# Optimization experiments

Hardware: AMD Instinct MI355X
Metric: run time of the kernel (lower is better)

The kernel has to match this reference:

```python
import jax, jax.numpy as jnp
import numpy as np

B, LQ, LK, E, H = 2, 1024, 10000, 256, 8
D = E // H  # head_dim = 32


def setup_inputs() -> dict:
    key = jax.random.key(0)
    ks = jax.random.split(key, 10)
    s = 1.0 / np.sqrt(E).astype(np.float32)
    return {
        "bev_emb": jax.random.normal(ks[0], (B, LK, E), jnp.float32),
        "queries": jax.random.normal(ks[1], (B, LQ, E), jnp.float32),
        "Wq": jax.random.normal(ks[2], (E, E), jnp.float32) * s,
        "bq": jax.random.normal(ks[3], (E,), jnp.float32) * 0.01,
        "Wk": jax.random.normal(ks[4], (E, E), jnp.float32) * s,
        "bk": jax.random.normal(ks[5], (E,), jnp.float32) * 0.01,
        "Wv": jax.random.normal(ks[6], (E, E), jnp.float32) * s,
        "bv": jax.random.normal(ks[7], (E,), jnp.float32) * 0.01,
        "Wo": jax.random.normal(ks[8], (E, E), jnp.float32) * s,
        "bo": jax.random.normal(ks[9], (E,), jnp.float32) * 0.01,
    }


def reference(bev_emb, queries, Wq, bq, Wk, bk, Wv, bv, Wo, bo):
    Bn, Lq, Em = queries.shape
    Lk = bev_emb.shape[1]
    q = (queries @ Wq + bq).reshape(Bn, Lq, H, D)
    k = (bev_emb @ Wk + bk).reshape(Bn, Lk, H, D)
    v = (bev_emb @ Wv + bv).reshape(Bn, Lk, H, D)
    # NOTE: source applies no 1/sqrt(head_dim) scaling
    energy = jnp.einsum('bqhd,bkhd->bhqk', q, k)  # [B,H,Lq,Lk]
    attn = jax.nn.softmax(energy, axis=-1)
    out = jnp.einsum('bhqk,bkhd->bqhd', attn, v).reshape(Bn, Lq, Em)
    return out @ Wo + bo
```

## Files before the change

### kernel.cpp

```cpp
#include <hip/hip_runtime.h>
#include <hip/hip_bf16.h>

#define B_  2
#define LQ_ 1024
#define LK_ 10000
#define E_  256
#define H_  8
#define D_  32
#define NT_ ((LK_ + 63) / 64)
#define KVBLKS_ 625
#define QBLKS_  64

typedef __attribute__((ext_vector_type(8))) short bf16x8;
typedef __attribute__((ext_vector_type(4))) short bf16x4;
typedef __attribute__((ext_vector_type(4))) float f32x4;

#define LOG2E 1.4426950408889634f

static __device__ __forceinline__ short bfc(float x) {
  __bf16 b = (__bf16)x;
  return __builtin_bit_cast(short, b);
}
static __device__ __forceinline__ float bf2f(short s) {
  return (float)__builtin_bit_cast(__bf16, s);
}

#if __has_builtin(__builtin_amdgcn_exp2f)
static __device__ __forceinline__ float ex2(float x) {
  return __builtin_amdgcn_exp2f(x);
}
#else
static __device__ __forceinline__ float ex2(float x) { return exp2f(x); }
#endif

#if __has_builtin(__builtin_amdgcn_mfma_f32_16x16x16bf16_1k)
static __device__ __forceinline__ f32x4 mfma_pv(bf16x4 a, bf16x4 b, f32x4 c) {
  return __builtin_amdgcn_mfma_f32_16x16x16bf16_1k(a, b, c, 0, 0, 0);
}
#else
static __device__ __forceinline__ f32x4 mfma_pv(bf16x4 a, bf16x4 b, f32x4 c) {
  asm volatile("s_nop 1\n\tv_mfma_f32_16x16x16_bf16 %0, %1, %2, %0"
               : "+v"(c) : "v"(a), "v"(b));
  return c;
}
#endif

static __device__ __forceinline__ void tile_barrier() {
  __builtin_amdgcn_sched_barrier(0);
  asm volatile("s_waitcnt lgkmcnt(0)" ::: "memory");
  __builtin_amdgcn_s_barrier();
  __builtin_amdgcn_sched_barrier(0);
}

static __device__ __forceinline__ int xcd_swizzle(int flat, int nwg) {
  const int xcd = flat & 7, rest = flat >> 3;
  const int q = nwg >> 3, r = nwg & 7;
  return (xcd < r ? xcd * (q + 1) : r * (q + 1) + (xcd - r) * q) + rest;
}

static __device__ __forceinline__ void split8(const float4& a, const float4& b,
                                              bf16x8& hi, bf16x8& lo) {
  float v[8] = {a.x, a.y, a.z, a.w, b.x, b.y, b.z, b.w};
#pragma unroll
  for (int i = 0; i < 8; ++i) {
    const short h = bfc(v[i]);
    hi[i] = h;
    lo[i] = bfc(v[i] - bf2f(h));
  }
}

__global__ __launch_bounds__(256) void wtrans4(
    const float* __restrict__ W0, const float* __restrict__ W1,
    const float* __restrict__ W2, const float* __restrict__ W3,
    unsigned short* __restrict__ T0, unsigned short* __restrict__ T1,
    unsigned short* __restrict__ T2, unsigned short* __restrict__ T3) {
  const float* W;
  unsigned short* T;
  switch (blockIdx.z) {
    case 0:  W = W0; T = T0; break;
    case 1:  W = W1; T = T1; break;
    case 2:  W = W2; T = T2; break;
    default: W = W3; T = T3; break;
  }
  __shared__ float ts[16][17];
  const int tx = threadIdx.x & 15;
  const int ty = threadIdx.x >> 4;
  const int k0 = blockIdx.x * 16;
  const int n0 = blockIdx.y * 16;
  ts[ty][tx] = W[(size_t)(k0 + ty) * 256 + n0 + tx];
  __syncthreads();
  T[(size_t)(n0 + ty) * 256 + k0 + tx] = (unsigned short)bfc(ts[tx][ty]);
}

__global__ __launch_bounds__(256) void proj_all(
    const float* __restrict__ bev, const float* __restrict__ queries,
    const unsigned short* __restrict__ Wtk, const unsigned short* __restrict__ Wtv,
    const unsigned short* __restrict__ Wtq,
    const float* __restrict__ bk, const float* __restrict__ bv,
    const float* __restrict__ bq,
    unsigned short* __restrict__ kout, unsigned short* __restrict__ vout,
    float* __restrict__ qout) {
  const int lane = threadIdx.x & 63;
  const int nt   = threadIdx.x >> 6;
  const int lr   = lane & 15;
  const int oc   = lane >> 4;
  const int n0   = nt * 64;

  const bool isQ = (blockIdx.x >= KVBLKS_);
  const int  m0  = (isQ ? (int)blockIdx.x - KVBLKS_ : (int)blockIdx.x) * 32;
  const float* A = isQ ? queries : bev;
  const unsigned short* W1 = isQ ? Wtq : Wtk;

  f32x4 ac1[2][4], ac2[2][4];
#pragma unroll
  for (int s = 0; s < 2; ++s)
#pragma unroll
    for (int q = 0; q < 4; ++q) {
      ac1[s][q] = (f32x4){0.f, 0.f, 0.f, 0.f};
      ac2[s][q] = (f32x4){0.f, 0.f, 0.f, 0.f};
    }

  const float* a0p = &A[(size_t)(m0 + lr) * 256 + oc * 8];
  const float* a1p = a0p + 16 * 256;

  float4 ab[3][4];
#pragma unroll
  for (int i = 0; i < 3; ++i) {
    ab[i][0] = *(const float4*)(a0p + i * 32 + 0);
    ab[i][1] = *(const float4*)(a0p + i * 32 + 4);
    ab[i][2] = *(const float4*)(a1p + i * 32 + 0);
    ab[i][3] = *(const float4*)(a1p + i * 32 + 4);
  }

#pragma unroll
  for (int kb = 0; kb < 8; ++kb) {
    const int bk_ = kb % 3;
    const int wko = kb * 32 + oc * 8;
    bf16x8 w1[4], w2[4];
#pragma unroll
    for (int q = 0; q < 4; ++q) {
      w1[q] = *(const bf16x8*)&W1[(size_t)(n0 + q * 16 + lr) * 256 + wko];
      if (!isQ) w2[q] = *(const bf16x8*)&Wtv[(size_t)(n0 + q * 16 + lr) * 256 + wko];
    }

    bf16x8 ah0, al0, ah1, al1;
    split8(ab[bk_][0], ab[bk_][1], ah0, al0);
    split8(ab[bk_][2], ab[bk_][3], ah1, al1);

    if (kb < 5) {
      ab[bk_][0] = *(const float4*)(a0p + (kb + 3) * 32 + 0);
      ab[bk_][1] = *(const float4*)(a0p + (kb + 3) * 32 + 4);
      ab[bk_][2] = *(const float4*)(a1p + (kb + 3) * 32 + 0);
      ab[bk_][3] = *(const float4*)(a1p + (kb + 3) * 32 + 4);
    }

#pragma unroll
    for (int q = 0; q < 4; ++q) {
      ac1[0][q] = __builtin_amdgcn_mfma_f32_16x16x32_bf16(w1[q], ah0, ac1[0][q], 0, 0, 0);
      ac1[0][q] = __builtin_amdgcn_mfma_f32_16x16x32_bf16(w1[q], al0, ac1[0][q], 0, 0, 0);
      ac1[1][q] = __builtin_amdgcn_mfma_f32_16x16x32_bf16(w1[q], ah1, ac1[1][q], 0, 0, 0);
      ac1[1][q] = __builtin_amdgcn_mfma_f32_16x16x32_bf16(w1[q], al1, ac1[1][q], 0, 0, 0);
      if (!isQ) {
        ac2[0][q] = __builtin_amdgcn_mfma_f32_16x16x32_bf16(w2[q], ah0, ac2[0][q], 0, 0, 0);
        ac2[1][q] = __builtin_amdgcn_mfma_f32_16x16x32_bf16(w2[q], ah1, ac2[1][q], 0, 0, 0);
      }
    }
  }

#pragma unroll
  for (int s = 0; s < 2; ++s) {
#pragma unroll
    for (int q = 0; q < 4; ++q) {
      const int m = m0 + s * 16 + lr;
      const int n = n0 + q * 16 + oc * 4;
      if (isQ) {
        const float4 b4 = *(const float4*)&bq[n];
        float4 o;
        o.x = ac1[s][q][0] + b4.x; o.y = ac1[s][q][1] + b4.y;
        o.z = ac1[s][q][2] + b4.z; o.w = ac1[s][q][3] + b4.w;
        *(float4*)&qout[(size_t)m * 256 + n] = o;
      } else {
        const float4 bk4 = *(const float4*)&bk[n];
        const float4 bv4 = *(const float4*)&bv[n];
        ushort4 ok, ov;
        ok.x = (unsigned short)bfc(ac1[s][q][0] + bk4.x);
        ok.y = (unsigned short)bfc(ac1[s][q][1] + bk4.y);
        ok.z = (unsigned short)bfc(ac1[s][q][2] + bk4.z);
        ok.w = (unsigned short)bfc(ac1[s][q][3] + bk4.w);
        ov.x = (unsigned short)bfc(ac2[s][q][0] + bv4.x);
        ov.y = (unsigned short)bfc(ac2[s][q][1] + bv4.y);
        ov.z = (unsigned short)bfc(ac2[s][q][2] + bv4.z);
        ov.w = (unsigned short)bfc(ac2[s][q][3] + bv4.w);
        *(ushort4*)&kout[(size_t)m * 256 + n] = ok;
        *(ushort4*)&vout[(size_t)m * 256 + n] = ov;
      }
    }
  }
}

__global__ __launch_bounds__(256) void proj_o(const float* __restrict__ A,
                                              const unsigned short* __restrict__ Wt,
                                              const float* __restrict__ bias,
                                              float* __restrict__ C) {
  const int lane = threadIdx.x & 63;
  const int nt   = threadIdx.x >> 6;
  const int lr   = lane & 15;
  const int oc   = lane >> 4;
  const int n0   = nt * 64;
  const int m0   = blockIdx.x * 32;

  f32x4 acc[2][4];
#pragma unroll
  for (int s = 0; s < 2; ++s)
#pragma unroll
    for (int q = 0; q < 4; ++q) acc[s][q] = (f32x4){0.f, 0.f, 0.f, 0.f};

  const float* a0p = &A[(size_t)(m0 + lr) * 256 + oc * 8];
  const float* a1p = a0p + 16 * 256;

  float4 ab[3][4];
#pragma unroll
  for (int i = 0; i < 3; ++i) {
    ab[i][0] = *(const float4*)(a0p + i * 32 + 0);
    ab[i][1] = *(const float4*)(a0p + i * 32 + 4);
    ab[i][2] = *(const float4*)(a1p + i * 32 + 0);
    ab[i][3] = *(const float4*)(a1p + i * 32 + 4);
  }

#pragma unroll
  for (int kb = 0; kb < 8; ++kb) {
    const int bk_ = kb % 3;
    const int wko = kb * 32 + oc * 8;
    bf16x8 w[4];
#pragma unroll
    for (int q = 0; q < 4; ++q)
      w[q] = *(const bf16x8*)&Wt[(size_t)(n0 + q * 16 + lr) * 256 + wko];

    bf16x8 ah0, al0, ah1, al1;
    split8(ab[bk_][0], ab[bk_][1], ah0, al0);
    split8(ab[bk_][2], ab[bk_][3], ah1, al1);

    if (kb < 5) {
      ab[bk_][0] = *(const float4*)(a0p + (kb + 3) * 32 + 0);
      ab[bk_][1] = *(const float4*)(a0p + (kb + 3) * 32 + 4);
      ab[bk_][2] = *(const float4*)(a1p + (kb + 3) * 32 + 0);
      ab[bk_][3] = *(const float4*)(a1p + (kb + 3) * 32 + 4);
    }

#pragma unroll
    for (int q = 0; q < 4; ++q) {
      acc[0][q] = __builtin_amdgcn_mfma_f32_16x16x32_bf16(w[q], ah0, acc[0][q], 0, 0, 0);
      acc[0][q] = __builtin_amdgcn_mfma_f32_16x16x32_bf16(w[q], al0, acc[0][q], 0, 0, 0);
      acc[1][q] = __builtin_amdgcn_mfma_f32_16x16x32_bf16(w[q], ah1, acc[1][q], 0, 0, 0);
      acc[1][q] = __builtin_amdgcn_mfma_f32_16x16x32_bf16(w[q], al1, acc[1][q], 0, 0, 0);
    }
  }

#pragma unroll
  for (int s = 0; s < 2; ++s) {
#pragma unroll
    for (int q = 0; q < 4; ++q) {
      const int m = m0 + s * 16 + lr;
      const int n = n0 + q * 16 + oc * 4;
      const float4 b4 = *(const float4*)&bias[n];
      float4 o;
      o.x = acc[s][q][0] + b4.x; o.y = acc[s][q][1] + b4.y;
      o.z = acc[s][q][2] + b4.z; o.w = acc[s][q][3] + b4.w;
      *(float4*)&C[(size_t)m * 256 + n] = o;
    }
  }
}

__global__ __launch_bounds__(256, 2) void attn_mfma(const float* __restrict__ q,
                                                    const unsigned short* __restrict__ kbf,
                                                    const unsigned short* __restrict__ vbf,
                                                    float* __restrict__ Opart,
                                                    float* __restrict__ lpart,
                                                    float* __restrict__ o_direct,
                                                    int tiles_per_split, int nsplit) {
  const int nwg = 32 * gridDim.z;
  const int l   = xcd_swizzle(blockIdx.x + 4 * (blockIdx.y + 8 * blockIdx.z), nwg);
  const int qb   = l & 3;
  const int h    = (l >> 2) & 7;
  const int z    = l >> 5;
  const int s_id = z / B_;
  const int b    = z % B_;
  const int t    = threadIdx.x;
  const int lane = t & 63;
  const int w    = t >> 6;
  const int lq   = lane & 15;
  const int grp  = lane >> 4;

  __shared__ ushort Klds[2][64][64];
  __shared__ ushort Vtld[2][32][64];

  const int t0 = s_id * tiles_per_split;
  const int t1 = min(NT_, t0 + tiles_per_split);
  if (t0 >= NT_) return;

  const int qrow0 = qb * 256 + w * 64 + lq;
  bf16x8 qf[4];
#pragma unroll
  for (int f = 0; f < 4; ++f) {
    const float* qp = &q[((size_t)(b * LQ_ + qrow0 + f * 16)) * E_ + h * D_ + grp * 8];
    const float4 x0 = *(const float4*)qp;
    const float4 x1 = *(const float4*)(qp + 4);
    qf[f][0] = bfc(x0.x * LOG2E); qf[f][1] = bfc(x0.y * LOG2E);
    qf[f][2] = bfc(x0.z * LOG2E); qf[f][3] = bfc(x0.w * LOG2E);
    qf[f][4] = bfc(x1.x * LOG2E); qf[f][5] = bfc(x1.y * LOG2E);
    qf[f][6] = bfc(x1.z * LOG2E); qf[f][7] = bfc(x1.w * LOG2E);
  }

  const int krow_l = t >> 2;
  const int kchunk = t & 3;
  const int vkp    = t >> 3;
  const int vd     = (t & 7) * 4;

  f32x4 lv[4];
  f32x4 acc0[4], acc1[4];
#pragma unroll
  for (int f = 0; f < 4; ++f) {
    lv[f]   = (f32x4){0.f, 0.f, 0.f, 0.f};
    acc0[f] = (f32x4){0.f, 0.f, 0.f, 0.f};
    acc1[f] = (f32x4){0.f, 0.f, 0.f, 0.f};
  }

  const size_t kvrow0 = (size_t)b * LK_;

  uint4 kval; ushort4 v0, v1;
  auto load_tile = [&](int kn) {
    if (kn == NT_ - 1) {
      const int krow  = min(kn * 64 + krow_l, LK_ - 1);
      const int vrow0 = min(kn * 64 + 2 * vkp, LK_ - 1);
      const int vrow1 = min(kn * 64 + 2 * vkp + 1, LK_ - 1);
      kval = *(const uint4*)&kbf[(kvrow0 + krow) * E_ + h * D_ + kchunk * 8];
      v0 = *(const ushort4*)&vbf[(kvrow0 + vrow0) * E_ + h * D_ + vd];
      v1 = *(const ushort4*)&vbf[(kvrow0 + vrow1) * E_ + h * D_ + vd];
    } else {
      kval = *(const uint4*)&kbf[(kvrow0 + kn * 64 + krow_l) * E_ + h * D_ + kchunk * 8];
      v0 = *(const ushort4*)&vbf[(kvrow0 + kn * 64 + 2 * vkp) * E_ + h * D_ + vd];
      v1 = *(const ushort4*)&vbf[(kvrow0 + kn * 64 + 2 * vkp + 1) * E_ + h * D_ + vd];
    }
  };
  auto store_tile = [&](int buf) {
    *(uint4*)((char*)&Klds[buf][krow_l][0] + ((kchunk * 16) ^ ((krow_l & 7) << 4))) = kval;
#pragma unroll
    for (int i = 0; i < 4; ++i) {
      const int d = vd + i;
      *(ushort2*)((char*)&Vtld[buf][d][0] + ((vkp * 4) ^ ((d & 7) << 4))) =
          make_ushort2(((const unsigned short*)&v0)[i], ((const unsigned short*)&v1)[i]);
    }
  };

  load_tile(t0);
  store_tile(0);
  if (t0 + 1 < t1) load_tile(t0 + 1);
  tile_barrier();

  int cur = 0;
  for (int kt = t0; kt < t1; ++kt) {
    const int rem = LK_ - kt * 64;

    if (kt + 1 < t1) store_tile(cur ^ 1);
    if (kt + 2 < t1) load_tile(kt + 2);

#pragma unroll
    for (int s = 0; s < 4; ++s) {
      const int row = s * 16 + lq;
      const bf16x8 kf = *(const bf16x8*)((const char*)&Klds[cur][row][0] +
                                         ((grp * 16) ^ ((row & 7) << 4)));
      const f32x4 zero = {0.f, 0.f, 0.f, 0.f};
      f32x4 p[4];
      __builtin_amdgcn_s_setprio(1);
#pragma unroll
      for (int f = 0; f < 4; ++f)
        p[f] = __builtin_amdgcn_mfma_f32_16x16x32_bf16(kf, qf[f], zero, 0, 0, 0);
      __builtin_amdgcn_s_setprio(0);

      bf16x4 pb[4];
      const bool vs = (rem >= 64) || (s * 16 + grp * 4 < rem);
#pragma unroll
      for (int f = 0; f < 4; ++f) {
#pragma unroll
        for (int r = 0; r < 4; ++r) {
          const float e = vs ? ex2(p[f][r]) : 0.f;
          lv[f][r] += e;
          pb[f][r] = bfc(e);
        }
      }

      const bf16x4 vfa = *(const bf16x4*)((const char*)&Vtld[cur][lq][0] +
                                          ((s * 32 + grp * 8) ^ ((lq & 7) << 4)));
      const bf16x4 vfb = *(const bf16x4*)((const char*)&Vtld[cur][16 + lq][0] +
                                          ((s * 32 + grp * 8) ^ (((16 + lq) & 7) << 4)));
      __builtin_amdgcn_s_setprio(1);
#pragma unroll
      for (int f = 0; f < 4; ++f) {
        acc0[f] = mfma_pv(vfa, pb[f], acc0[f]);
        acc1[f] = mfma_pv(vfb, pb[f], acc1[f]);
      }
      __builtin_amdgcn_s_setprio(0);
    }

    tile_barrier();
    cur ^= 1;
  }

  float lsc[4];
#pragma unroll
  for (int f = 0; f < 4; ++f) {
    float x = (lv[f][0] + lv[f][1]) + (lv[f][2] + lv[f][3]);
    x += __shfl_xor(x, 16);
    x += __shfl_xor(x, 32);
    lsc[f] = x;
  }

  if (nsplit == 1) {
#pragma unroll
    for (int f = 0; f < 4; ++f) {
      const float inv = 1.f / lsc[f];
      float* op = &o_direct[((size_t)(b * LQ_ + qrow0 + f * 16)) * E_ + h * D_];
#pragma unroll
      for (int r = 0; r < 4; ++r) {
        op[grp * 4 + r]      = acc0[f][r] * inv;
        op[16 + grp * 4 + r] = acc1[f][r] * inv;
      }
    }
  } else {
#pragma unroll
    for (int f = 0; f < 4; ++f) {
      const size_t pb_ = (size_t)s_id * (B_ * H_ * LQ_) +
                         ((size_t)b * H_ + h) * LQ_ + qrow0 + f * 16;
#pragma unroll
      for (int r = 0; r < 4; ++r) {
        Opart[pb_ * D_ + grp * 4 + r]      = acc0[f][r];
        Opart[pb_ * D_ + 16 + grp * 4 + r] = acc1[f][r];
      }
      if (grp == 0) lpart[pb_] = lsc[f];
    }
  }
}

__global__ __launch_bounds__(256) void attn_merge(const float* __restrict__ Opart,
                                                  const float* __restrict__ lpart,
                                                  float* __restrict__ o, int S) {
  const int idx = blockIdx.x * 256 + threadIdx.x;
  if (idx >= B_ * LQ_ * E_) return;
  const int e   = idx & (E_ - 1);
  const int row = idx >> 8;
  const int b   = row >> 10;
  const int qq  = row & (LQ_ - 1);
  const int h   = e >> 5;
  const int d   = e & (D_ - 1);
  const size_t base   = ((size_t)b * H_ + h) * LQ_ + qq;
  const size_t stride = (size_t)B_ * H_ * LQ_;

  float lsum = 0.f, osum = 0.f;
  for (int s = 0; s < S; ++s) {
    lsum += lpart[s * stride + base];
    osum += Opart[(s * stride + base) * D_ + d];
  }
  o[idx] = osum / lsum;
}

extern "C" void kernel_launch(void* const* d_in, const int* in_sizes, int n_in,
                              void* d_out, int out_size, void* d_ws, size_t ws_size,
                              hipStream_t stream) {
  const float* bev     = (const float*)d_in[0];
  const float* queries = (const float*)d_in[1];
  const float* Wq      = (const float*)d_in[2];
  const float* bq      = (const float*)d_in[3];
  const float* Wk      = (const float*)d_in[4];
  const float* bk      = (const float*)d_in[5];
  const float* Wv      = (const float*)d_in[6];
  const float* bv      = (const float*)d_in[7];
  const float* Wo      = (const float*)d_in[8];
  const float* bo      = (const float*)d_in[9];
  float* out = (float*)d_out;

  const size_t nq = (size_t)B_ * LQ_ * E_;
  const size_t nk = (size_t)B_ * LK_ * E_;
  const size_t nw = (size_t)E_ * E_;
  float*          qws = (float*)d_ws;
  unsigned short* kbf = (unsigned short*)(qws + nq);
  unsigned short* vbf = kbf + nk;
  float*          ows = (float*)(vbf + nk);
  unsigned short* Wtq = (unsigned short*)(ows + nq);
  unsigned short* Wtk = Wtq + nw;
  unsigned short* Wtv = Wtk + nw;
  unsigned short* Wto = Wtv + nw;
  float*          opart = (float*)(Wto + nw);

  const size_t base_bytes = (nq * 2) * sizeof(float) +
                            (nk * 2 + nw * 4) * sizeof(unsigned short);
  const size_t per_split_bytes = (size_t)B_ * H_ * LQ_ * (D_ + 1) * sizeof(float);
  const int cands[4] = {8, 4, 2, 1};
  int S = 1;
  for (int ci = 0; ci < 4; ++ci) {
    if (base_bytes + (size_t)cands[ci] * per_split_bytes <= ws_size) {
      S = cands[ci];
      break;
    }
  }

  wtrans4<<<dim3(16, 16, 4), 256, 0, stream>>>(Wq, Wk, Wv, Wo, Wtq, Wtk, Wtv, Wto);

  proj_all<<<dim3(KVBLKS_ + QBLKS_), 256, 0, stream>>>(
      bev, queries, Wtk, Wtv, Wtq, bk, bv, bq, kbf, vbf, qws);

  if (S <= 1) {
    attn_mfma<<<dim3(4, H_, B_), 256, 0, stream>>>(
        qws, kbf, vbf, nullptr, nullptr, ows, NT_, 1);
  } else {
    float* lpart = opart + (size_t)S * B_ * H_ * LQ_ * D_;
    const int tps = (NT_ + S - 1) / S;
    attn_mfma<<<dim3(4, H_, B_ * S), 256, 0, stream>>>(
        qws, kbf, vbf, opart, lpart, nullptr, tps, S);
    attn_merge<<<dim3((B_ * LQ_ * E_ + 255) / 256), 256, 0, stream>>>(
        opart, lpart, ows, S);
  }

  proj_o<<<dim3(QBLKS_), 256, 0, stream>>>(ows, Wto, bo, out);
}
```

Before: 117.0 us.

## Split attention KV tile across wave pairs and double the query-block grid

The attention kernel now uses 128-row query blocks. Its four waves are split into two query halves by two key halves, so each wave processes half of every 64-key tile, and the partial accumulators and row sums are combined through shared memory at the end. The grid doubles to give more workgroups, and launch bounds ask for four workgroups per CU to raise occupancy. The two projection kernels also shrink their A-operand prefetch ring from three stages to two, which lowers register use. In exchange, each workgroup loads the same K/V tiles for only half as many queries, so K/V traffic per query rises, and the reduction adds an extra barrier step.

```diff
diff --git a/kernel.cpp b/kernel.cpp
--- a/kernel.cpp
+++ b/kernel.cpp
@@ -123,18 +123,20 @@
   const float* a0p = &A[(size_t)(m0 + lr) * 256 + oc * 8];
   const float* a1p = a0p + 16 * 256;
 
-  float4 ab[3][4];
-#pragma unroll
-  for (int i = 0; i < 3; ++i) {
-    ab[i][0] = *(const float4*)(a0p + i * 32 + 0);
-    ab[i][1] = *(const float4*)(a0p + i * 32 + 4);
-    ab[i][2] = *(const float4*)(a1p + i * 32 + 0);
-    ab[i][3] = *(const float4*)(a1p + i * 32 + 4);
-  }
+  float4 ab[2][4];
+  ab[0][0] = *(const float4*)(a0p + 0);
+  ab[0][1] = *(const float4*)(a0p + 4);
+  ab[0][2] = *(const float4*)(a1p + 0);
+  ab[0][3] = *(const float4*)(a1p + 4);
+  ab[1][0] = *(const float4*)(a0p + 32);
+  ab[1][1] = *(const float4*)(a0p + 36);
+  ab[1][2] = *(const float4*)(a1p + 32);
+  ab[1][3] = *(const float4*)(a1p + 36);
 
 #pragma unroll
   for (int kb = 0; kb < 8; ++kb) {
-    const int bk_ = kb % 3;
+    const int bk_ = kb & 1;
+
     const int wko = kb * 32 + oc * 8;
     bf16x8 w1[4], w2[4];
 #pragma unroll
@@ -147,11 +149,11 @@
     split8(ab[bk_][0], ab[bk_][1], ah0, al0);
     split8(ab[bk_][2], ab[bk_][3], ah1, al1);
 
-    if (kb < 5) {
-      ab[bk_][0] = *(const float4*)(a0p + (kb + 3) * 32 + 0);
-      ab[bk_][1] = *(const float4*)(a0p + (kb + 3) * 32 + 4);
-      ab[bk_][2] = *(const float4*)(a1p + (kb + 3) * 32 + 0);
-      ab[bk_][3] = *(const float4*)(a1p + (kb + 3) * 32 + 4);
+    if (kb < 6) {
+      ab[bk_][0] = *(const float4*)(a0p + (kb + 2) * 32 + 0);
+      ab[bk_][1] = *(const float4*)(a0p + (kb + 2) * 32 + 4);
+      ab[bk_][2] = *(const float4*)(a1p + (kb + 2) * 32 + 0);
+      ab[bk_][3] = *(const float4*)(a1p + (kb + 2) * 32 + 4);
     }
 
 #pragma unroll
@@ -218,18 +220,19 @@
   const float* a0p = &A[(size_t)(m0 + lr) * 256 + oc * 8];
   const float* a1p = a0p + 16 * 256;
 
-  float4 ab[3][4];
-#pragma unroll
-  for (int i = 0; i < 3; ++i) {
-    ab[i][0] = *(const float4*)(a0p + i * 32 + 0);
-    ab[i][1] = *(const float4*)(a0p + i * 32 + 4);
-    ab[i][2] = *(const float4*)(a1p + i * 32 + 0);
-    ab[i][3] = *(const float4*)(a1p + i * 32 + 4);
-  }
+  float4 ab[2][4];
+  ab[0][0] = *(const float4*)(a0p + 0);
+  ab[0][1] = *(const float4*)(a0p + 4);
+  ab[0][2] = *(const float4*)(a1p + 0);
+  ab[0][3] = *(const float4*)(a1p + 4);
+  ab[1][0] = *(const float4*)(a0p + 32);
+  ab[1][1] = *(const float4*)(a0p + 36);
+  ab[1][2] = *(const float4*)(a1p + 32);
+  ab[1][3] = *(const float4*)(a1p + 36);
 
 #pragma unroll
   for (int kb = 0; kb < 8; ++kb) {
-    const int bk_ = kb % 3;
+    const int bk_ = kb & 1;
     const int wko = kb * 32 + oc * 8;
     bf16x8 w[4];
 #pragma unroll
@@ -240,11 +243,11 @@
     split8(ab[bk_][0], ab[bk_][1], ah0, al0);
     split8(ab[bk_][2], ab[bk_][3], ah1, al1);
 
-    if (kb < 5) {
-      ab[bk_][0] = *(const float4*)(a0p + (kb + 3) * 32 + 0);
-      ab[bk_][1] = *(const float4*)(a0p + (kb + 3) * 32 + 4);
-      ab[bk_][2] = *(const float4*)(a1p + (kb + 3) * 32 + 0);
-      ab[bk_][3] = *(const float4*)(a1p + (kb + 3) * 32 + 4);
+    if (kb < 6) {
+      ab[bk_][0] = *(const float4*)(a0p + (kb + 2) * 32 + 0);
+      ab[bk_][1] = *(const float4*)(a0p + (kb + 2) * 32 + 4);
+      ab[bk_][2] = *(const float4*)(a1p + (kb + 2) * 32 + 0);
+      ab[bk_][3] = *(const float4*)(a1p + (kb + 2) * 32 + 4);
     }
 
 #pragma unroll
@@ -271,38 +274,42 @@
   }
 }
 
-__global__ __launch_bounds__(256, 2) void attn_mfma(const float* __restrict__ q,
+__global__ __launch_bounds__(256, 4) void attn_mfma(const float* __restrict__ q,
                                                     const unsigned short* __restrict__ kbf,
                                                     const unsigned short* __restrict__ vbf,
                                                     float* __restrict__ Opart,
                                                     float* __restrict__ lpart,
                                                     float* __restrict__ o_direct,
                                                     int tiles_per_split, int nsplit) {
-  const int nwg = 32 * gridDim.z;
-  const int l   = xcd_swizzle(blockIdx.x + 4 * (blockIdx.y + 8 * blockIdx.z), nwg);
-  const int qb   = l & 3;
-  const int h    = (l >> 2) & 7;
-  const int z    = l >> 5;
+  const int nwg = 64 * gridDim.z;
+  const int l   = xcd_swizzle(blockIdx.x + 8 * (blockIdx.y + 8 * blockIdx.z), nwg);
+  const int qb   = l & 7;
+  const int h    = (l >> 3) & 7;
+  const int z    = l >> 6;
   const int s_id = z / B_;
   const int b    = z % B_;
   const int t    = threadIdx.x;
   const int lane = t & 63;
   const int w    = t >> 6;
+  const int qh   = w >> 1;
+  const int kh   = w & 1;
   const int lq   = lane & 15;
   const int grp  = lane >> 4;
 
-  __shared__ ushort Klds[2][64][64];
-  __shared__ ushort Vtld[2][32][64];
+  __shared__ __align__(16) char shraw[24576];
+  typedef ushort KT[64][64];
+  typedef ushort VT[32][64];
+  KT* Klds = (KT*)shraw;
+  VT* Vtld = (VT*)(shraw + 16384);
 
   const int t0 = s_id * tiles_per_split;
   const int t1 = min(NT_, t0 + tiles_per_split);
-  if (t0 >= NT_) return;
-
-  const int qrow0 = qb * 256 + w * 64 + lq;
+
+  const int qbase = qb * 128 + qh * 64 + lq;
   bf16x8 qf[4];
 #pragma unroll
   for (int f = 0; f < 4; ++f) {
-    const float* qp = &q[((size_t)(b * LQ_ + qrow0 + f * 16)) * E_ + h * D_ + grp * 8];
+    const float* qp = &q[((size_t)(b * LQ_ + qbase + f * 16)) * E_ + h * D_ + grp * 8];
     const float4 x0 = *(const float4*)qp;
     const float4 x1 = *(const float4*)(qp + 4);
     qf[f][0] = bfc(x0.x * LOG2E); qf[f][1] = bfc(x0.y * LOG2E);
@@ -317,12 +324,12 @@
   const int vd     = (t & 7) * 4;
 
   f32x4 lv[4];
-  f32x4 acc0[4], acc1[4];
+  f32x4 accL[4], accH[4];
 #pragma unroll
   for (int f = 0; f < 4; ++f) {
     lv[f]   = (f32x4){0.f, 0.f, 0.f, 0.f};
-    acc0[f] = (f32x4){0.f, 0.f, 0.f, 0.f};
-    acc1[f] = (f32x4){0.f, 0.f, 0.f, 0.f};
+    accL[f] = (f32x4){0.f, 0.f, 0.f, 0.f};
+    accH[f] = (f32x4){0.f, 0.f, 0.f, 0.f};
   }
 
   const size_t kvrow0 = (size_t)b * LK_;
@@ -365,20 +372,22 @@
     if (kt + 2 < t1) load_tile(kt + 2);
 
 #pragma unroll
-    for (int s = 0; s < 4; ++s) {
-      const int row = s * 16 + lq;
+    for (int s = 0; s < 2; ++s) {
+      const int ss  = kh * 2 + s;
+      const int row = ss * 16 + lq;
       const bf16x8 kf = *(const bf16x8*)((const char*)&Klds[cur][row][0] +
                                          ((grp * 16) ^ ((row & 7) << 4)));
-      const f32x4 zero = {0.f, 0.f, 0.f, 0.f};
       f32x4 p[4];
       __builtin_amdgcn_s_setprio(1);
 #pragma unroll
-      for (int f = 0; f < 4; ++f)
+      for (int f = 0; f < 4; ++f) {
+        const f32x4 zero = {0.f, 0.f, 0.f, 0.f};
         p[f] = __builtin_amdgcn_mfma_f32_16x16x32_bf16(kf, qf[f], zero, 0, 0, 0);
+      }
       __builtin_amdgcn_s_setprio(0);
 
+      const bool vs = (rem >= 64) || (ss * 16 + grp * 4 < rem);
       bf16x4 pb[4];
-      const bool vs = (rem >= 64) || (s * 16 + grp * 4 < rem);
 #pragma unroll
       for (int f = 0; f < 4; ++f) {
 #pragma unroll
@@ -390,14 +399,14 @@
       }
 
       const bf16x4 vfa = *(const bf16x4*)((const char*)&Vtld[cur][lq][0] +
-                                          ((s * 32 + grp * 8) ^ ((lq & 7) << 4)));
+                                          ((ss * 32 + grp * 8) ^ ((lq & 7) << 4)));
       const bf16x4 vfb = *(const bf16x4*)((const char*)&Vtld[cur][16 + lq][0] +
-                                          ((s * 32 + grp * 8) ^ (((16 + lq) & 7) << 4)));
+                                          ((ss * 32 + grp * 8) ^ (((16 + lq) & 7) << 4)));
       __builtin_amdgcn_s_setprio(1);
 #pragma unroll
       for (int f = 0; f < 4; ++f) {
-        acc0[f] = mfma_pv(vfa, pb[f], acc0[f]);
-        acc1[f] = mfma_pv(vfb, pb[f], acc1[f]);
+        accL[f] = mfma_pv(vfa, pb[f], accL[f]);
+        accH[f] = mfma_pv(vfb, pb[f], accH[f]);
       }
       __builtin_amdgcn_s_setprio(0);
     }
@@ -406,37 +415,58 @@
     cur ^= 1;
   }
 
-  float lsc[4];
+  float lf[4];
 #pragma unroll
   for (int f = 0; f < 4; ++f) {
     float x = (lv[f][0] + lv[f][1]) + (lv[f][2] + lv[f][3]);
     x += __shfl_xor(x, 16);
     x += __shfl_xor(x, 32);
-    lsc[f] = x;
-  }
-
-  if (nsplit == 1) {
+    lf[f] = x;
+  }
+
+  __syncthreads();
+  float* red = (float*)shraw;
+  if (kh == 1) {
 #pragma unroll
     for (int f = 0; f < 4; ++f) {
-      const float inv = 1.f / lsc[f];
-      float* op = &o_direct[((size_t)(b * LQ_ + qrow0 + f * 16)) * E_ + h * D_];
-#pragma unroll
-      for (int r = 0; r < 4; ++r) {
-        op[grp * 4 + r]      = acc0[f][r] * inv;
-        op[16 + grp * 4 + r] = acc1[f][r] * inv;
-      }
-    }
-  } else {
+      float* rp = &red[(size_t)(((qh * 4 + f) * 64 + lane) * 9)];
+      rp[0] = accL[f][0]; rp[1] = accL[f][1]; rp[2] = accL[f][2]; rp[3] = accL[f][3];
+      rp[4] = accH[f][0]; rp[5] = accH[f][1]; rp[6] = accH[f][2]; rp[7] = accH[f][3];
+      rp[8] = lf[f];
+    }
+  }
+  __syncthreads();
+  if (kh == 0) {
 #pragma unroll
     for (int f = 0; f < 4; ++f) {
-      const size_t pb_ = (size_t)s_id * (B_ * H_ * LQ_) +
-                         ((size_t)b * H_ + h) * LQ_ + qrow0 + f * 16;
-#pragma unroll
-      for (int r = 0; r < 4; ++r) {
-        Opart[pb_ * D_ + grp * 4 + r]      = acc0[f][r];
-        Opart[pb_ * D_ + 16 + grp * 4 + r] = acc1[f][r];
-      }
-      if (grp == 0) lpart[pb_] = lsc[f];
+      const float* rp = &red[(size_t)(((qh * 4 + f) * 64 + lane) * 9)];
+      accL[f][0] += rp[0]; accL[f][1] += rp[1]; accL[f][2] += rp[2]; accL[f][3] += rp[3];
+      accH[f][0] += rp[4]; accH[f][1] += rp[5]; accH[f][2] += rp[6]; accH[f][3] += rp[7];
+      lf[f] += rp[8];
+    }
+    if (nsplit == 1) {
+#pragma unroll
+      for (int f = 0; f < 4; ++f) {
+        const float inv = 1.f / lf[f];
+        float* op = &o_direct[((size_t)(b * LQ_ + qbase + f * 16)) * E_ + h * D_];
+#pragma unroll
+        for (int r = 0; r < 4; ++r) {
+          op[grp * 4 + r]      = accL[f][r] * inv;
+          op[16 + grp * 4 + r] = accH[f][r] * inv;
+        }
+      }
+    } else {
+#pragma unroll
+      for (int f = 0; f < 4; ++f) {
+        const size_t pb_ = (size_t)s_id * (B_ * H_ * LQ_) +
+                           ((size_t)b * H_ + h) * LQ_ + qbase + f * 16;
+#pragma unroll
+        for (int r = 0; r < 4; ++r) {
+          Opart[pb_ * D_ + grp * 4 + r]      = accL[f][r];
+          Opart[pb_ * D_ + 16 + grp * 4 + r] = accH[f][r];
+        }
+        if (grp == 0) lpart[pb_] = lf[f];
+      }
     }
   }
 }
@@ -509,12 +539,12 @@
       bev, queries, Wtk, Wtv, Wtq, bk, bv, bq, kbf, vbf, qws);
 
   if (S <= 1) {
-    attn_mfma<<<dim3(4, H_, B_), 256, 0, stream>>>(
+    attn_mfma<<<dim3(8, H_, B_), 256, 0, stream>>>(
         qws, kbf, vbf, nullptr, nullptr, ows, NT_, 1);
   } else {
     float* lpart = opart + (size_t)S * B_ * H_ * LQ_ * D_;
     const int tps = (NT_ + S - 1) / S;
-    attn_mfma<<<dim3(4, H_, B_ * S), 256, 0, stream>>>(
+    attn_mfma<<<dim3(8, H_, B_ * S), 256, 0, stream>>>(
         qws, kbf, vbf, opart, lpart, nullptr, tps, S);
     attn_merge<<<dim3((B_ * LQ_ * E_ + 255) / 256), 256, 0, stream>>>(
         opart, lpart, ows, S);
```

New measurement: 116.8 us. Within noise of the previous version (-0.1%).
